# Kernel optimization log

Measured on AMD Instinct MI355X. Metric: run time of the kernel, lower is better.

The kernel has to match this reference:

```python
import jax, jax.numpy as jnp
import numpy as np

N_NODES = 100000
N_EDGES = 1600000
N_GRAPHS = 128
DIM = 64
N_LAYERS = 4
DENSE = 256
BN_EPS = 1e-5


def setup_inputs() -> dict:
    key = jax.random.key(0)
    ks = list(jax.random.split(key, 24))
    k = iter(ks)
    def lin(kk, fan_in, shape):
        b = 1.0 / np.sqrt(fan_in)
        return jax.random.uniform(kk, shape, jnp.float32, -b, b)
    inp = {}
    inp['x'] = jax.random.normal(next(k), (N_NODES, 32), jnp.float32)
    inp['edge_attr'] = jax.random.normal(next(k), (N_EDGES, 16), jnp.float32)
    inp['edge_index'] = jax.random.randint(next(k), (2, N_EDGES), 0, N_NODES, jnp.int32)
    inp['batch'] = jnp.sort(jax.random.randint(next(k), (N_NODES,), 0, N_GRAPHS, jnp.int32))
    # encoders
    inp['node_W'] = lin(next(k), 32, (32, DIM)); inp['node_b'] = lin(next(k), 32, (DIM,))
    inp['edge_W'] = lin(next(k), 16, (16, DIM)); inp['edge_b'] = lin(next(k), 16, (DIM,))
    # per-layer GINE MLPs (stacked over layer dim) and BN affine params
    inp['mlp1_W'] = lin(next(k), DIM, (N_LAYERS, DIM, DIM)); inp['mlp1_b'] = lin(next(k), DIM, (N_LAYERS, DIM))
    inp['mlp2_W'] = lin(next(k), DIM, (N_LAYERS, DIM, DIM)); inp['mlp2_b'] = lin(next(k), DIM, (N_LAYERS, DIM))
    inp['bn_gamma'] = jnp.ones((N_LAYERS, DIM), jnp.float32)
    inp['bn_beta'] = jnp.zeros((N_LAYERS, DIM), jnp.float32)
    # head: Linear(128,256) -> Linear(256,128) -> Linear(128,1)
    inp['head1_W'] = lin(next(k), 2 * DIM, (2 * DIM, DENSE)); inp['head1_b'] = lin(next(k), 2 * DIM, (DENSE,))
    inp['head2_W'] = lin(next(k), DENSE, (DENSE, DENSE // 2)); inp['head2_b'] = lin(next(k), DENSE, (DENSE // 2,))
    inp['head3_W'] = lin(next(k), DENSE // 2, (DENSE // 2, 1)); inp['head3_b'] = lin(next(k), DENSE // 2, (1,))
    return inp


def reference(x, edge_attr, edge_index, batch, node_W, node_b, edge_W, edge_b,
              mlp1_W, mlp1_b, mlp2_W, mlp2_b, bn_gamma, bn_beta,
              head1_W, head1_b, head2_W, head2_b, head3_W, head3_b):
    src, dst = edge_index[0], edge_index[1]  # messages flow src (x_j) -> dst (x_i)
    h = x @ node_W + node_b                  # [N, DIM]
    e = edge_attr @ edge_W + edge_b          # [E, DIM]
    for l in range(N_LAYERS):
        # GINEConv (eps = 0, not trained): mlp((1+eps)*x_i + sum_j relu(x_j + e_ij))
        msg = jax.nn.relu(h[src] + e)                              # [E, DIM]
        agg = jax.ops.segment_sum(msg, dst, num_segments=N_NODES)  # [N, DIM]
        z = h + agg
        z = jax.nn.relu(z @ mlp1_W[l] + mlp1_b[l]) @ mlp2_W[l] + mlp2_b[l]
        # BatchNorm1d (training-mode batch statistics, biased variance)
        mu = jnp.mean(z, axis=0)
        var = jnp.mean(jnp.square(z - mu), axis=0)
        z = (z - mu) * jax.lax.rsqrt(var + BN_EPS) * bn_gamma[l] + bn_beta[l]
        h = jax.nn.relu(z)
    sums = jax.ops.segment_sum(h, batch, num_segments=N_GRAPHS)                      # [G, DIM]
    counts = jax.ops.segment_sum(jnp.ones((h.shape[0],), h.dtype), batch, num_segments=N_GRAPHS)
    means = sums / jnp.maximum(counts, 1.0)[:, None]
    g = jnp.concatenate([sums, means], axis=1)   # [G, 2*DIM]
    g = jax.nn.relu(g @ head1_W + head1_b)       # dropout is identity at inference
    g = jax.nn.relu(g @ head2_W + head2_b)
    logits = (g @ head3_W + head3_b).reshape(-1) # [G]
    return logits
```

## Files before the change

### kernel.cpp

```cpp
#include <hip/hip_runtime.h>

#define SCAN_B 1024
#define NGRAPH 128
typedef unsigned short u16;
typedef unsigned int u32;
typedef u32 u32x2 __attribute__((ext_vector_type(2)));
typedef u32 u32x4 __attribute__((ext_vector_type(4)));
typedef float fx4 __attribute__((ext_vector_type(4)));
typedef _Float16 f16;
typedef _Float16 f16x2 __attribute__((ext_vector_type(2)));
typedef _Float16 f16x8 __attribute__((ext_vector_type(8)));
typedef float f32x4 __attribute__((ext_vector_type(4)));

__device__ __forceinline__ u16 f2h(float f) {
  f16 h = (f16)f;
  return __builtin_bit_cast(u16, h);
}
__device__ __forceinline__ float h2f(u16 u) {
  return (float)__builtin_bit_cast(f16, u);
}
__device__ __forceinline__ float hlo(u32 w) { return h2f((u16)(w & 0xffffu)); }
__device__ __forceinline__ float hhi(u32 w) { return h2f((u16)(w >> 16)); }

__device__ __forceinline__ void bn4(const float* __restrict__ stat,
                                    const float* __restrict__ gamma,
                                    const float* __restrict__ beta,
                                    float invN, int c4,
                                    float4& sc4, float4& sh4)
{
  float4 s1 = *(const float4*)&stat[c4];
  float4 s2 = *(const float4*)&stat[64 + c4];
  float4 g4 = *(const float4*)&gamma[c4];
  float4 b4 = *(const float4*)&beta[c4];
#define BN1(k)                                                        \
  { float mu = s1.k * invN;                                           \
    float var = fmaxf(s2.k * invN - mu * mu, 0.f);                    \
    sc4.k = g4.k * rsqrtf(var + 1e-5f);                               \
    sh4.k = b4.k - mu * sc4.k; }
  BN1(x) BN1(y) BN1(z) BN1(w)
#undef BN1
}

__global__ __launch_bounds__(256) void node_enc_kernel(
    const float* __restrict__ x, const float* __restrict__ W,
    const float* __restrict__ b, u16* __restrict__ zh, int N)
{
  int lane = threadIdx.x & 63;
  int wave = (blockIdx.x * blockDim.x + threadIdx.x) >> 6;
  int nw = (gridDim.x * blockDim.x) >> 6;
  float wcol[32];
#pragma unroll
  for (int k = 0; k < 32; ++k) wcol[k] = W[k * 64 + lane];
  float bb = b[lane];
  for (int n = wave; n < N; n += nw) {
    const fx4* xr = (const fx4*)(x + (size_t)n * 32);
    float acc = bb;
#pragma unroll
    for (int c = 0; c < 8; ++c) {
      fx4 v = __builtin_nontemporal_load(&xr[c]);
      acc = fmaf(v[0], wcol[4 * c + 0], acc);
      acc = fmaf(v[1], wcol[4 * c + 1], acc);
      acc = fmaf(v[2], wcol[4 * c + 2], acc);
      acc = fmaf(v[3], wcol[4 * c + 3], acc);
    }
    zh[(size_t)n * 64 + lane] = f2h(acc);
  }
}

__global__ __launch_bounds__(256) void count_pos_kernel(
    const int* __restrict__ dst, int* __restrict__ deg,
    int* __restrict__ pos, int E)
{
  int e = blockIdx.x * blockDim.x + threadIdx.x;
  if (e < E) pos[e] = atomicAdd(&deg[dst[e]], 1);
}

__global__ __launch_bounds__(SCAN_B) void scan1_kernel(
    const int* __restrict__ deg, int* __restrict__ rowp,
    int* __restrict__ bsum, int N)
{
  __shared__ int s[SCAN_B];
  int tid = threadIdx.x;
  int i = blockIdx.x * SCAN_B + tid;
  int v = (i < N) ? deg[i] : 0;
  s[tid] = v;
  __syncthreads();
  for (int off = 1; off < SCAN_B; off <<= 1) {
    int t = (tid >= off) ? s[tid - off] : 0;
    __syncthreads();
    s[tid] += t;
    __syncthreads();
  }
  if (i < N) rowp[i] = s[tid] - v;
  if (tid == SCAN_B - 1) bsum[blockIdx.x] = s[tid];
}

__global__ __launch_bounds__(128) void scan2_kernel(int* __restrict__ bsum, int NB)
{
  __shared__ int s[128];
  int tid = threadIdx.x;
  int v = (tid < NB) ? bsum[tid] : 0;
  s[tid] = v;
  __syncthreads();
  for (int off = 1; off < 128; off <<= 1) {
    int t = (tid >= off) ? s[tid - off] : 0;
    __syncthreads();
    s[tid] += t;
    __syncthreads();
  }
  if (tid < NB) bsum[tid] = s[tid] - v;
}

__global__ __launch_bounds__(SCAN_B) void scan3_kernel(
    int* __restrict__ rowp, const int* __restrict__ bsum, int N, int E)
{
  int i = blockIdx.x * SCAN_B + threadIdx.x;
  if (i < N) rowp[i] += bsum[blockIdx.x];
  if (i == 0) rowp[N] = E;
}

__global__ __launch_bounds__(256) void scatter_pos_kernel(
    const int* __restrict__ dst, const int* __restrict__ rowp,
    const int* __restrict__ pos, int* __restrict__ eids, int E)
{
  int e = blockIdx.x * blockDim.x + threadIdx.x;
  if (e >= E) return;
  int p = rowp[dst[e]] + pos[e];
  eids[p] = e;
}

__global__ __launch_bounds__(256) void scatter_e_kernel(
    const int* __restrict__ dst, const int* __restrict__ src,
    const int* __restrict__ pos, const fx4* __restrict__ attr4,
    const int* __restrict__ rowp, const float* __restrict__ eW,
    const float* __restrict__ eb_, int* __restrict__ src_s,
    u16* __restrict__ e_s, int E)
{
  int lane = threadIdx.x & 63;
  int c = lane & 15, q = lane >> 4;
  int wave = (blockIdx.x * blockDim.x + threadIdx.x) >> 6;
  int base = wave << 6;
  if (base >= E) return;
  int nb = E - base; if (nb > 64) nb = 64;

  float wcol[4][16];
#pragma unroll
  for (int ch = 0; ch < 4; ++ch)
#pragma unroll
    for (int k = 0; k < 16; ++k)
      wcol[ch][k] = eW[k * 64 + 4 * c + ch];
  float4 eb4 = *(const float4*)&eb_[4 * c];

  int pv = 0;
  if (lane < nb) {
    int e = base + lane;
    pv = rowp[dst[e]] + pos[e];
    src_s[pv] = src[e];
  }

  auto enc = [&](fx4 a0, fx4 a1, fx4 a2, fx4 a3, int slot) {
    float m0 = eb4.x, m1 = eb4.y, m2 = eb4.z, m3 = eb4.w;
#define ESTEP(av, k)                                                   \
    m0 = fmaf(av, wcol[0][k], m0); m1 = fmaf(av, wcol[1][k], m1);      \
    m2 = fmaf(av, wcol[2][k], m2); m3 = fmaf(av, wcol[3][k], m3);
    ESTEP(a0[0], 0)  ESTEP(a0[1], 1)  ESTEP(a0[2], 2)  ESTEP(a0[3], 3)
    ESTEP(a1[0], 4)  ESTEP(a1[1], 5)  ESTEP(a1[2], 6)  ESTEP(a1[3], 7)
    ESTEP(a2[0], 8)  ESTEP(a2[1], 9)  ESTEP(a2[2], 10) ESTEP(a2[3], 11)
    ESTEP(a3[0], 12) ESTEP(a3[1], 13) ESTEP(a3[2], 14) ESTEP(a3[3], 15)
#undef ESTEP
    u32x2 o;
    o[0] = (u32)f2h(m0) | ((u32)f2h(m1) << 16);
    o[1] = (u32)f2h(m2) | ((u32)f2h(m3) << 16);
    *(u32x2*)(e_s + (size_t)slot * 64 + 4 * c) = o;
  };

  if (nb == 64) {
#pragma unroll 2
    for (int t = 0; t < 16; t += 2) {
      int pA = __shfl(pv, 4 * t + q, 64);
      int pB = __shfl(pv, 4 * t + 4 + q, 64);
      const fx4* rA = attr4 + (size_t)(base + 4 * t + q) * 4;
      const fx4* rB = attr4 + (size_t)(base + 4 * t + 4 + q) * 4;
      fx4 A0 = __builtin_nontemporal_load(rA);
      fx4 A1 = __builtin_nontemporal_load(rA + 1);
      fx4 A2 = __builtin_nontemporal_load(rA + 2);
      fx4 A3 = __builtin_nontemporal_load(rA + 3);
      fx4 B0 = __builtin_nontemporal_load(rB);
      fx4 B1 = __builtin_nontemporal_load(rB + 1);
      fx4 B2 = __builtin_nontemporal_load(rB + 2);
      fx4 B3 = __builtin_nontemporal_load(rB + 3);
      enc(A0, A1, A2, A3, pA);
      enc(B0, B1, B2, B3, pB);
    }
  } else {
    for (int t = 0; 4 * t < nb; ++t) {
      int idx = 4 * t + q;
      int p = __shfl(pv, idx < nb ? idx : 0, 64);
      if (idx < nb) {
        const fx4* rA = attr4 + (size_t)(base + idx) * 4;
        fx4 A0 = rA[0], A1 = rA[1], A2 = rA[2], A3 = rA[3];
        enc(A0, A1, A2, A3, p);
      }
    }
  }
}

__global__ __launch_bounds__(256) void prep_weights_kernel(
    const float* __restrict__ mlp1_W, const float* __restrict__ mlp2_W,
    u16* __restrict__ Wt)
{
  int idx = blockIdx.x * 256 + threadIdx.x;
  if (idx >= 32768) return;
  int layer = idx >> 13;
  int which = (idx >> 12) & 1;
  int d = (idx >> 6) & 63;
  int k = idx & 63;
  const float* W = which ? mlp2_W : mlp1_W;
  Wt[idx] = f2h(W[layer * 4096 + k * 64 + d]);
}

__global__ __launch_bounds__(256, 4) void gather_kernel(
    const u16* __restrict__ zh, const float* __restrict__ stat_rd,
    const float* __restrict__ gamma, const float* __restrict__ beta,
    float invN, float* __restrict__ stat_wr,
    const u16* __restrict__ e_s, const int* __restrict__ srcv,
    const int* __restrict__ rowp, u16* __restrict__ gh, int N)
{
  if (blockIdx.x == 0 && threadIdx.x < 128) stat_wr[threadIdx.x] = 0.f;

  int lane = threadIdx.x & 63;
  int c = lane & 15, q = lane >> 4;
  int wave = (blockIdx.x * blockDim.x + threadIdx.x) >> 6;
  int nw = (gridDim.x * blockDim.x) >> 6;

  const bool ubn = stat_rd != nullptr;
  float4 sc4 = make_float4(1.f, 1.f, 1.f, 1.f);
  float4 sh4 = make_float4(0.f, 0.f, 0.f, 0.f);
  if (ubn) bn4(stat_rd, gamma, beta, invN, 4 * c, sc4, sh4);

  auto hval4 = [&](u32x2 z, float& h0, float& h1, float& h2, float& h3) {
    h0 = hlo(z[0]); h1 = hhi(z[0]); h2 = hlo(z[1]); h3 = hhi(z[1]);
    if (ubn) {
      h0 = fmaxf(fmaf(h0, sc4.x, sh4.x), 0.f);
      h1 = fmaxf(fmaf(h1, sc4.y, sh4.y), 0.f);
      h2 = fmaxf(fmaf(h2, sc4.z, sh4.z), 0.f);
      h3 = fmaxf(fmaf(h3, sc4.w, sh4.w), 0.f);
    }
  };
  auto body = [&](u32x2 z, u32x2 e,
                  float& A0, float& A1, float& A2, float& A3) {
    float h0, h1, h2, h3;
    hval4(z, h0, h1, h2, h3);
    A0 += fmaxf(h0 + hlo(e[0]), 0.f);
    A1 += fmaxf(h1 + hhi(e[0]), 0.f);
    A2 += fmaxf(h2 + hlo(e[1]), 0.f);
    A3 += fmaxf(h3 + hhi(e[1]), 0.f);
  };

  for (int node = wave; node < N; node += nw) {
    const int j0 = rowp[node], j1 = rowp[node + 1];
    float acc0 = 0.f, acc1 = 0.f, acc2 = 0.f, acc3 = 0.f;

    for (int base = j0; base < j1; base += 64) {
      int nb = j1 - base; if (nb > 64) nb = 64;
      int iv = (lane < nb) ? srcv[base + lane] : 0;
      int ng = nb >> 2;
      int t = 0;
      for (; t + 4 <= ng; t += 4) {
        int s0 = __shfl(iv, 4 * t + q, 64);
        int s1 = __shfl(iv, 4 * t + 4 + q, 64);
        int s2 = __shfl(iv, 4 * t + 8 + q, 64);
        int s3 = __shfl(iv, 4 * t + 12 + q, 64);
        u32x2 z0 = *(const u32x2*)(zh + (size_t)s0 * 64 + 4 * c);
        u32x2 z1 = *(const u32x2*)(zh + (size_t)s1 * 64 + 4 * c);
        u32x2 z2 = *(const u32x2*)(zh + (size_t)s2 * 64 + 4 * c);
        u32x2 z3 = *(const u32x2*)(zh + (size_t)s3 * 64 + 4 * c);
        u32x2 e0 = *(const u32x2*)(e_s + (size_t)(base + 4 * t + q) * 64 + 4 * c);
        u32x2 e1 = *(const u32x2*)(e_s + (size_t)(base + 4 * t + 4 + q) * 64 + 4 * c);
        u32x2 e2 = *(const u32x2*)(e_s + (size_t)(base + 4 * t + 8 + q) * 64 + 4 * c);
        u32x2 e3 = *(const u32x2*)(e_s + (size_t)(base + 4 * t + 12 + q) * 64 + 4 * c);
        body(z0, e0, acc0, acc1, acc2, acc3);
        body(z1, e1, acc0, acc1, acc2, acc3);
        body(z2, e2, acc0, acc1, acc2, acc3);
        body(z3, e3, acc0, acc1, acc2, acc3);
      }
      for (; t < ng; ++t) {
        int s0 = __shfl(iv, 4 * t + q, 64);
        u32x2 z0 = *(const u32x2*)(zh + (size_t)s0 * 64 + 4 * c);
        u32x2 e0 = *(const u32x2*)(e_s + (size_t)(base + 4 * t + q) * 64 + 4 * c);
        body(z0, e0, acc0, acc1, acc2, acc3);
      }
      int tail = nb & 3;
      if (tail) {
        int idx = 4 * ng + (q < tail ? q : 0);
        int s0 = __shfl(iv, idx, 64);
        u32x2 z0 = *(const u32x2*)(zh + (size_t)s0 * 64 + 4 * c);
        u32x2 e0 = *(const u32x2*)(e_s + (size_t)(base + idx) * 64 + 4 * c);
        float h0, h1, h2, h3;
        hval4(z0, h0, h1, h2, h3);
        float wmask = (q < tail) ? 1.f : 0.f;
        acc0 += wmask * fmaxf(h0 + hlo(e0[0]), 0.f);
        acc1 += wmask * fmaxf(h1 + hhi(e0[0]), 0.f);
        acc2 += wmask * fmaxf(h2 + hlo(e0[1]), 0.f);
        acc3 += wmask * fmaxf(h3 + hhi(e0[1]), 0.f);
      }
    }
    acc0 += __shfl_xor(acc0, 16, 64); acc0 += __shfl_xor(acc0, 32, 64);
    acc1 += __shfl_xor(acc1, 16, 64); acc1 += __shfl_xor(acc1, 32, 64);
    acc2 += __shfl_xor(acc2, 16, 64); acc2 += __shfl_xor(acc2, 32, 64);
    acc3 += __shfl_xor(acc3, 16, 64); acc3 += __shfl_xor(acc3, 32, 64);
    if (q == 0) {
      u32x2 zn = *(const u32x2*)(zh + (size_t)node * 64 + 4 * c);
      float h0, h1, h2, h3;
      hval4(zn, h0, h1, h2, h3);
      acc0 += h0; acc1 += h1; acc2 += h2; acc3 += h3;
      u32x2 o;
      o[0] = (u32)f2h(acc0) | ((u32)f2h(acc1) << 16);
      o[1] = (u32)f2h(acc2) | ((u32)f2h(acc3) << 16);
      *(u32x2*)(gh + (size_t)node * 64 + 4 * c) = o;
    }
  }
}

__global__ __launch_bounds__(256) void gather_fallback_kernel(
    const u16* __restrict__ zh, const float* __restrict__ stat_rd,
    const float* __restrict__ gamma, const float* __restrict__ beta,
    float invN, float* __restrict__ stat_wr,
    const int* __restrict__ srcv, const int* __restrict__ eids,
    const int* __restrict__ rowp, const float* __restrict__ attr,
    const float* __restrict__ eW, const float* __restrict__ eb_,
    u16* __restrict__ gh, int N)
{
  if (blockIdx.x == 0 && threadIdx.x < 128) stat_wr[threadIdx.x] = 0.f;
  int lane = threadIdx.x & 63;
  int node = (blockIdx.x * blockDim.x + threadIdx.x) >> 6;
  if (node >= N) return;
  const bool ubn = stat_rd != nullptr;
  float sc = 1.f, sh = 0.f;
  if (ubn) {
    float mu = stat_rd[lane] * invN;
    float var = fmaxf(stat_rd[64 + lane] * invN - mu * mu, 0.f);
    sc = gamma[lane] * rsqrtf(var + 1e-5f);
    sh = beta[lane] - mu * sc;
  }
  auto hval = [&](float zz) -> float {
    float v = fmaf(zz, sc, sh);
    return ubn ? fmaxf(v, 0.f) : v;
  };
  float wcol[16];
#pragma unroll
  for (int k = 0; k < 16; ++k) wcol[k] = eW[k * 64 + lane];
  float eb = eb_[lane];
  const int j0 = rowp[node], j1 = rowp[node + 1];
  float acc = hval(h2f(zh[(size_t)node * 64 + lane]));
  for (int j = j0; j < j1; ++j) {
    int eid = eids[j];
    int s = srcv[j];
    const float4* ar = (const float4*)(attr + (size_t)eid * 16);
    float4 a0 = ar[0], a1 = ar[1], a2 = ar[2], a3 = ar[3];
    float m = eb;
    m = fmaf(a0.x, wcol[0], m);  m = fmaf(a0.y, wcol[1], m);
    m = fmaf(a0.z, wcol[2], m);  m = fmaf(a0.w, wcol[3], m);
    m = fmaf(a1.x, wcol[4], m);  m = fmaf(a1.y, wcol[5], m);
    m = fmaf(a1.z, wcol[6], m);  m = fmaf(a1.w, wcol[7], m);
    m = fmaf(a2.x, wcol[8], m);  m = fmaf(a2.y, wcol[9], m);
    m = fmaf(a2.z, wcol[10], m); m = fmaf(a2.w, wcol[11], m);
    m = fmaf(a3.x, wcol[12], m); m = fmaf(a3.y, wcol[13], m);
    m = fmaf(a3.z, wcol[14], m); m = fmaf(a3.w, wcol[15], m);
    acc += fmaxf(hval(h2f(zh[(size_t)s * 64 + lane])) + m, 0.f);
  }
  gh[(size_t)node * 64 + lane] = f2h(acc);
}

__global__ __launch_bounds__(256) void mlp_mfma_kernel(
    const u16* __restrict__ gh, u16* __restrict__ zh,
    const u16* __restrict__ W1t, const u16* __restrict__ W2t,
    const float* __restrict__ b1, const float* __restrict__ b2,
    float* __restrict__ stat, int N)
{
  __shared__ __align__(16) u16 ylds[4][16][72];
  __shared__ float sstat[128];
  int tid = threadIdx.x, lane = tid & 63, w = tid >> 6;
  int l15 = lane & 15, lg = lane >> 4;
  int row_base = (blockIdx.x * 4 + w) * 32;

  if (tid < 128) sstat[tid] = 0.f;
  __syncthreads();

  f16x8 w1f[2][4], w2f[2][4];
#pragma unroll
  for (int ks = 0; ks < 2; ++ks)
#pragma unroll
    for (int nt = 0; nt < 4; ++nt) {
      int off = (nt * 16 + l15) * 64 + ks * 32 + lg * 8;
      w1f[ks][nt] = *(const f16x8*)&W1t[off];
      w2f[ks][nt] = *(const f16x8*)&W2t[off];
    }
  float bv1[4], bv2[4];
#pragma unroll
  for (int nt = 0; nt < 4; ++nt) {
    bv1[nt] = b1[nt * 16 + l15];
    bv2[nt] = b2[nt * 16 + l15];
  }

  float s1acc[4] = {0.f, 0.f, 0.f, 0.f};
  float s2acc[4] = {0.f, 0.f, 0.f, 0.f};

#pragma unroll
  for (int tile = 0; tile < 2; ++tile) {
    int grow0 = row_base + tile * 16;
    int arow = grow0 + l15; if (arow >= N) arow = N - 1;
    const u16* grow = gh + (size_t)arow * 64;
    f16x8 a0 = *(const f16x8*)(grow + lg * 8);
    f16x8 a1 = *(const f16x8*)(grow + 32 + lg * 8);

    f32x4 c1[4];
#pragma unroll
    for (int nt = 0; nt < 4; ++nt) {
      c1[nt] = (f32x4){0.f, 0.f, 0.f, 0.f};
      c1[nt] = __builtin_amdgcn_mfma_f32_16x16x32_f16(a0, w1f[0][nt], c1[nt], 0, 0, 0);
      c1[nt] = __builtin_amdgcn_mfma_f32_16x16x32_f16(a1, w1f[1][nt], c1[nt], 0, 0, 0);
    }
#pragma unroll
    for (int nt = 0; nt < 4; ++nt)
#pragma unroll
      for (int r = 0; r < 4; ++r)
        ylds[w][lg * 4 + r][nt * 16 + l15] = f2h(fmaxf(c1[nt][r] + bv1[nt], 0.f));
    f16x8 a20 = *(const f16x8*)&ylds[w][l15][lg * 8];
    f16x8 a21 = *(const f16x8*)&ylds[w][l15][32 + lg * 8];

    f32x4 c2[4];
#pragma unroll
    for (int nt = 0; nt < 4; ++nt) {
      c2[nt] = (f32x4){0.f, 0.f, 0.f, 0.f};
      c2[nt] = __builtin_amdgcn_mfma_f32_16x16x32_f16(a20, w2f[0][nt], c2[nt], 0, 0, 0);
      c2[nt] = __builtin_amdgcn_mfma_f32_16x16x32_f16(a21, w2f[1][nt], c2[nt], 0, 0, 0);
    }
#pragma unroll
    for (int nt = 0; nt < 4; ++nt) {
#pragma unroll
      for (int r = 0; r < 4; ++r) {
        int row = grow0 + lg * 4 + r;
        float v = c2[nt][r] + bv2[nt];
        bool ok = row < N;
        if (ok) zh[(size_t)row * 64 + nt * 16 + l15] = f2h(v);
        float vm = ok ? v : 0.f;
        s1acc[nt] += vm;
        s2acc[nt] = fmaf(vm, vm, s2acc[nt]);
      }
    }
  }

#pragma unroll
  for (int nt = 0; nt < 4; ++nt) {
    float s1 = s1acc[nt], s2 = s2acc[nt];
    s1 += __shfl_xor(s1, 16, 64); s1 += __shfl_xor(s1, 32, 64);
    s2 += __shfl_xor(s2, 16, 64); s2 += __shfl_xor(s2, 32, 64);
    if (lg == 0) {
      atomicAdd(&sstat[nt * 16 + l15], s1);
      atomicAdd(&sstat[64 + nt * 16 + l15], s2);
    }
  }
  __syncthreads();
  if (tid < 128) atomicAdd(&stat[tid], sstat[tid]);
}

__global__ __launch_bounds__(256) void pool_kernel(
    const u16* __restrict__ zh, const float* __restrict__ stat_rd,
    const float* __restrict__ gamma, const float* __restrict__ beta,
    float invN, const int* __restrict__ batch,
    float* __restrict__ sums, float* __restrict__ cnts, int N)
{
  int lane = threadIdx.x & 63;
  int wave = (blockIdx.x * blockDim.x + threadIdx.x) >> 6;
  int r0 = wave * 64;
  if (r0 >= N) return;
  float mu = stat_rd[lane] * invN;
  float var = fmaxf(stat_rd[64 + lane] * invN - mu * mu, 0.f);
  float sc = gamma[lane] * rsqrtf(var + 1e-5f);
  float sh = beta[lane] - mu * sc;
  int r1 = min(r0 + 64, N);
  int cur = batch[r0];
  float acc = 0.f;
  int cnt = 0;
  for (int r = r0; r < r1; ++r) {
    int bg = batch[r];
    if (bg != cur) {
      atomicAdd(&sums[(size_t)cur * 64 + lane], acc);
      if (lane == 0) atomicAdd(&cnts[cur], (float)cnt);
      acc = 0.f; cnt = 0; cur = bg;
    }
    acc += fmaxf(fmaf(h2f(zh[(size_t)r * 64 + lane]), sc, sh), 0.f);
    cnt++;
  }
  atomicAdd(&sums[(size_t)cur * 64 + lane], acc);
  if (lane == 0) atomicAdd(&cnts[cur], (float)cnt);
}

__global__ __launch_bounds__(256) void head_kernel(
    const float* __restrict__ sums, const float* __restrict__ cnts,
    const float* __restrict__ W1, const float* __restrict__ b1,
    const float* __restrict__ W2, const float* __restrict__ b2,
    const float* __restrict__ W3, const float* __restrict__ b3,
    float* __restrict__ out)
{
  __shared__ float gf[128];
  __shared__ float h1s[256];
  __shared__ float h2s[128];
  int g = blockIdx.x, t = threadIdx.x;
  if (t < 64) {
    float sv = sums[(size_t)g * 64 + t];
    gf[t] = sv;
    gf[64 + t] = sv / fmaxf(cnts[g], 1.f);
  }
  __syncthreads();
  float a = b1[t];
  for (int k = 0; k < 128; ++k) a = fmaf(gf[k], W1[k * 256 + t], a);
  h1s[t] = fmaxf(a, 0.f);
  __syncthreads();
  if (t < 128) {
    float a2 = b2[t];
    for (int k = 0; k < 256; ++k) a2 = fmaf(h1s[k], W2[k * 128 + t], a2);
    h2s[t] = fmaxf(a2, 0.f);
  }
  __syncthreads();
  if (t == 0) {
    float s = b3[0];
    for (int k = 0; k < 128; ++k) s = fmaf(h2s[k], W3[k], s);
    out[g] = s;
  }
}

extern "C" void kernel_launch(void* const* d_in, const int* in_sizes, int n_in,
                              void* d_out, int out_size, void* d_ws, size_t ws_size,
                              hipStream_t stream)
{
  const float* x         = (const float*)d_in[0];
  const float* edge_attr = (const float*)d_in[1];
  const int*   ei        = (const int*)  d_in[2];
  const int*   batch     = (const int*)  d_in[3];
  const float* node_W    = (const float*)d_in[4];
  const float* node_b    = (const float*)d_in[5];
  const float* edge_W    = (const float*)d_in[6];
  const float* edge_b    = (const float*)d_in[7];
  const float* mlp1_W    = (const float*)d_in[8];
  const float* mlp1_b    = (const float*)d_in[9];
  const float* mlp2_W    = (const float*)d_in[10];
  const float* mlp2_b    = (const float*)d_in[11];
  const float* bn_gamma  = (const float*)d_in[12];
  const float* bn_beta   = (const float*)d_in[13];
  const float* head1_W   = (const float*)d_in[14];
  const float* head1_b   = (const float*)d_in[15];
  const float* head2_W   = (const float*)d_in[16];
  const float* head2_b   = (const float*)d_in[17];
  const float* head3_W   = (const float*)d_in[18];
  const float* head3_b   = (const float*)d_in[19];
  float* out = (float*)d_out;
  (void)n_in; (void)out_size;

  const int N = in_sizes[0] / 32;
  const int E = in_sizes[2] / 2;
  const int* srcp = ei;
  const int* dstp = ei + E;

  auto al = [](size_t b) { return (b + 255) & ~(size_t)255; };
  const size_t sz_zh   = al((size_t)N * 64 * 2);
  const size_t sz_g    = al((size_t)N * 64 * 2);
  const size_t sz_es   = al((size_t)E * 64 * 2);
  const size_t sz_src  = al((size_t)E * 4);
  const size_t sz_pos  = al((size_t)E * 4);
  const size_t sz_eids = al((size_t)E * 4);
  const size_t sz_rowp = al((size_t)(N + 1) * 4);
  const size_t sz_wt   = al(32768 * 2);
  const size_t sz_scr  = al((size_t)N * 4);
  const size_t sz_small = al(512) * 3 + al(NGRAPH * 64 * 4) + al(NGRAPH * 4);

  const size_t need_sorted = sz_zh + sz_g + sz_es + sz_src + sz_pos +
                             sz_eids + sz_rowp + sz_wt + sz_scr + sz_small;
  const bool sorted = ws_size >= need_sorted;

  char* p = (char*)d_ws;
  auto take = [&](size_t b) -> char* { char* q = p; p += b; return q; };

  u16*   zh   = (u16*)  take(sz_zh);
  u16*   gh   = (u16*)  take(sz_g);
  int*   rowp = (int*)  take(sz_rowp);
  u16*   Wt   = (u16*)  take(sz_wt);
  float* statA= (float*)take(al(512));
  float* statB= (float*)take(al(512));
  int*   bsum = (int*)  take(al(512));
  float* sums = (float*)take(al(NGRAPH * 64 * 4));
  float* cnts = (float*)take(al(NGRAPH * 4));
  int*   deg  = (int*)  take(sz_scr);
  int*   pos  = (int*)  take(sz_pos);
  int*   eids = (int*)  take(sz_eids);
  int*   src_s= (int*)  take(sz_src);

  u16* e_s = nullptr;
  if (sorted) e_s = (u16*)take(sz_es);

  const int NB = (N + SCAN_B - 1) / SCAN_B;
  const float invN = 1.0f / (float)N;
  float* statbuf[2] = {statA, statB};

  hipMemsetAsync(deg, 0, (size_t)N * 4, stream);

  node_enc_kernel<<<2048, 256, 0, stream>>>(x, node_W, node_b, zh, N);
  prep_weights_kernel<<<128, 256, 0, stream>>>(mlp1_W, mlp2_W, Wt);
  count_pos_kernel<<<(E + 255) / 256, 256, 0, stream>>>(dstp, deg, pos, E);
  scan1_kernel<<<NB, SCAN_B, 0, stream>>>(deg, rowp, bsum, N);
  scan2_kernel<<<1, 128, 0, stream>>>(bsum, NB);
  scan3_kernel<<<NB, SCAN_B, 0, stream>>>(rowp, bsum, N, E);
  if (sorted) {
    scatter_e_kernel<<<(E + 255) / 256, 256, 0, stream>>>(
        dstp, srcp, pos, (const fx4*)edge_attr, rowp, edge_W, edge_b,
        src_s, e_s, E);
  } else {
    scatter_pos_kernel<<<(E + 255) / 256, 256, 0, stream>>>(
        dstp, rowp, pos, eids, E);
    scatter_e_kernel<<<(E + 255) / 256, 256, 0, stream>>>(
        dstp, srcp, pos, (const fx4*)edge_attr, rowp, edge_W, edge_b,
        src_s, nullptr, E);
  }

  const int mlpBlocks = (N + 127) / 128;
  for (int l = 0; l < 4; ++l) {
    const float* stat_rd = (l == 0) ? nullptr : statbuf[(l - 1) & 1];
    float* stat_wr = statbuf[l & 1];
    const float* gma = bn_gamma + (size_t)(l ? (l - 1) : 0) * 64;
    const float* bta = bn_beta + (size_t)(l ? (l - 1) : 0) * 64;
    if (sorted) {
      gather_kernel<<<4096, 256, 0, stream>>>(
          zh, stat_rd, gma, bta, invN, stat_wr, e_s, src_s, rowp, gh, N);
    } else {
      gather_fallback_kernel<<<(N + 3) / 4, 256, 0, stream>>>(
          zh, stat_rd, gma, bta, invN, stat_wr, src_s, eids, rowp,
          edge_attr, edge_W, edge_b, gh, N);
    }
    mlp_mfma_kernel<<<mlpBlocks, 256, 0, stream>>>(
        gh, zh, Wt + (size_t)l * 8192, Wt + (size_t)l * 8192 + 4096,
        mlp1_b + (size_t)l * 64, mlp2_b + (size_t)l * 64, stat_wr, N);
  }

  hipMemsetAsync(sums, 0, (size_t)NGRAPH * 64 * 4, stream);
  hipMemsetAsync(cnts, 0, (size_t)NGRAPH * 4, stream);
  const int poolWaves = (N + 63) / 64;
  pool_kernel<<<(poolWaves + 3) / 4, 256, 0, stream>>>(
      zh, statbuf[1], bn_gamma + 3 * 64, bn_beta + 3 * 64, invN,
      batch, sums, cnts, N);
  head_kernel<<<NGRAPH, 256, 0, stream>>>(
      sums, cnts, head1_W, head1_b, head2_W, head2_b, head3_W, head3_b, out);
}
```

Measured before the change: 739.0 us.

## Store encoded edges in natural order and gather them via sorted (src, eid) pairs

Encoded edge features are now written in original edge order by a coalesced encode kernel, instead of being scattered into dst-sorted slots. A separate kernel scatters (src, edge id) pairs into CSR order. The gather kernel then reads edge features indirectly through the edge id. This makes the one-time encode write contiguous, but turns the per-layer edge-feature reads, run four times, from contiguous streaming into random 128-byte row gathers. It also doubles the size of the index array read in each layer.

New measurement: 733.3 us. No clear change (-0.8%).

```diff
diff --git a/kernel.cpp b/kernel.cpp
--- a/kernel.cpp
+++ b/kernel.cpp
@@ -7,8 +7,8 @@
 typedef u32 u32x2 __attribute__((ext_vector_type(2)));
 typedef u32 u32x4 __attribute__((ext_vector_type(4)));
 typedef float fx4 __attribute__((ext_vector_type(4)));
+typedef int ix2 __attribute__((ext_vector_type(2)));
 typedef _Float16 f16;
-typedef _Float16 f16x2 __attribute__((ext_vector_type(2)));
 typedef _Float16 f16x8 __attribute__((ext_vector_type(8)));
 typedef float f32x4 __attribute__((ext_vector_type(4)));
 
@@ -119,29 +119,27 @@
   if (i == 0) rowp[N] = E;
 }
 
-__global__ __launch_bounds__(256) void scatter_pos_kernel(
-    const int* __restrict__ dst, const int* __restrict__ rowp,
-    const int* __restrict__ pos, int* __restrict__ eids, int E)
+__global__ __launch_bounds__(256) void scatter_pairs_kernel(
+    const int* __restrict__ dst, const int* __restrict__ src,
+    const int* __restrict__ pos, const int* __restrict__ rowp,
+    ix2* __restrict__ pairs, int E)
 {
   int e = blockIdx.x * blockDim.x + threadIdx.x;
   if (e >= E) return;
   int p = rowp[dst[e]] + pos[e];
-  eids[p] = e;
-}
-
-__global__ __launch_bounds__(256) void scatter_e_kernel(
-    const int* __restrict__ dst, const int* __restrict__ src,
-    const int* __restrict__ pos, const fx4* __restrict__ attr4,
-    const int* __restrict__ rowp, const float* __restrict__ eW,
-    const float* __restrict__ eb_, int* __restrict__ src_s,
-    u16* __restrict__ e_s, int E)
+  ix2 v; v[0] = src[e]; v[1] = e;
+  pairs[p] = v;
+}
+
+__global__ __launch_bounds__(256) void encode_kernel(
+    const fx4* __restrict__ attr4, const float* __restrict__ eW,
+    const float* __restrict__ eb_, u16* __restrict__ e_nat, int E)
 {
   int lane = threadIdx.x & 63;
   int c = lane & 15, q = lane >> 4;
   int wave = (blockIdx.x * blockDim.x + threadIdx.x) >> 6;
   int base = wave << 6;
   if (base >= E) return;
-  int nb = E - base; if (nb > 64) nb = 64;
 
   float wcol[4][16];
 #pragma unroll
@@ -151,14 +149,7 @@
       wcol[ch][k] = eW[k * 64 + 4 * c + ch];
   float4 eb4 = *(const float4*)&eb_[4 * c];
 
-  int pv = 0;
-  if (lane < nb) {
-    int e = base + lane;
-    pv = rowp[dst[e]] + pos[e];
-    src_s[pv] = src[e];
-  }
-
-  auto enc = [&](fx4 a0, fx4 a1, fx4 a2, fx4 a3, int slot) {
+  auto enc = [&](fx4 a0, fx4 a1, fx4 a2, fx4 a3, int edge) {
     float m0 = eb4.x, m1 = eb4.y, m2 = eb4.z, m3 = eb4.w;
 #define ESTEP(av, k)                                                   \
     m0 = fmaf(av, wcol[0][k], m0); m1 = fmaf(av, wcol[1][k], m1);      \
@@ -171,35 +162,28 @@
     u32x2 o;
     o[0] = (u32)f2h(m0) | ((u32)f2h(m1) << 16);
     o[1] = (u32)f2h(m2) | ((u32)f2h(m3) << 16);
-    *(u32x2*)(e_s + (size_t)slot * 64 + 4 * c) = o;
+    *(u32x2*)(e_nat + (size_t)edge * 64 + 4 * c) = o;
   };
 
+  int nb = E - base; if (nb > 64) nb = 64;
   if (nb == 64) {
 #pragma unroll 2
-    for (int t = 0; t < 16; t += 2) {
-      int pA = __shfl(pv, 4 * t + q, 64);
-      int pB = __shfl(pv, 4 * t + 4 + q, 64);
-      const fx4* rA = attr4 + (size_t)(base + 4 * t + q) * 4;
-      const fx4* rB = attr4 + (size_t)(base + 4 * t + 4 + q) * 4;
+    for (int t = 0; t < 16; ++t) {
+      int edge = base + 4 * t + q;
+      const fx4* rA = attr4 + (size_t)edge * 4;
       fx4 A0 = __builtin_nontemporal_load(rA);
       fx4 A1 = __builtin_nontemporal_load(rA + 1);
       fx4 A2 = __builtin_nontemporal_load(rA + 2);
       fx4 A3 = __builtin_nontemporal_load(rA + 3);
-      fx4 B0 = __builtin_nontemporal_load(rB);
-      fx4 B1 = __builtin_nontemporal_load(rB + 1);
-      fx4 B2 = __builtin_nontemporal_load(rB + 2);
-      fx4 B3 = __builtin_nontemporal_load(rB + 3);
-      enc(A0, A1, A2, A3, pA);
-      enc(B0, B1, B2, B3, pB);
+      enc(A0, A1, A2, A3, edge);
     }
   } else {
     for (int t = 0; 4 * t < nb; ++t) {
-      int idx = 4 * t + q;
-      int p = __shfl(pv, idx < nb ? idx : 0, 64);
-      if (idx < nb) {
-        const fx4* rA = attr4 + (size_t)(base + idx) * 4;
+      int edge = base + 4 * t + q;
+      if (edge < E && 4 * t + q < nb) {
+        const fx4* rA = attr4 + (size_t)edge * 4;
         fx4 A0 = rA[0], A1 = rA[1], A2 = rA[2], A3 = rA[3];
-        enc(A0, A1, A2, A3, p);
+        enc(A0, A1, A2, A3, edge);
       }
     }
   }
@@ -223,7 +207,7 @@
     const u16* __restrict__ zh, const float* __restrict__ stat_rd,
     const float* __restrict__ gamma, const float* __restrict__ beta,
     float invN, float* __restrict__ stat_wr,
-    const u16* __restrict__ e_s, const int* __restrict__ srcv,
+    const u16* __restrict__ e_nat, const ix2* __restrict__ pairs,
     const int* __restrict__ rowp, u16* __restrict__ gh, int N)
 {
   if (blockIdx.x == 0 && threadIdx.x < 128) stat_wr[threadIdx.x] = 0.f;
@@ -263,39 +247,47 @@
 
     for (int base = j0; base < j1; base += 64) {
       int nb = j1 - base; if (nb > 64) nb = 64;
-      int iv = (lane < nb) ? srcv[base + lane] : 0;
+      ix2 iv = {0, 0};
+      if (lane < nb) iv = pairs[base + lane];
+      int sv = iv[0], dv = iv[1];
       int ng = nb >> 2;
       int t = 0;
       for (; t + 4 <= ng; t += 4) {
-        int s0 = __shfl(iv, 4 * t + q, 64);
-        int s1 = __shfl(iv, 4 * t + 4 + q, 64);
-        int s2 = __shfl(iv, 4 * t + 8 + q, 64);
-        int s3 = __shfl(iv, 4 * t + 12 + q, 64);
+        int s0 = __shfl(sv, 4 * t + q, 64);
+        int s1 = __shfl(sv, 4 * t + 4 + q, 64);
+        int s2 = __shfl(sv, 4 * t + 8 + q, 64);
+        int s3 = __shfl(sv, 4 * t + 12 + q, 64);
+        int d0 = __shfl(dv, 4 * t + q, 64);
+        int d1 = __shfl(dv, 4 * t + 4 + q, 64);
+        int d2 = __shfl(dv, 4 * t + 8 + q, 64);
+        int d3 = __shfl(dv, 4 * t + 12 + q, 64);
         u32x2 z0 = *(const u32x2*)(zh + (size_t)s0 * 64 + 4 * c);
         u32x2 z1 = *(const u32x2*)(zh + (size_t)s1 * 64 + 4 * c);
         u32x2 z2 = *(const u32x2*)(zh + (size_t)s2 * 64 + 4 * c);
         u32x2 z3 = *(const u32x2*)(zh + (size_t)s3 * 64 + 4 * c);
-        u32x2 e0 = *(const u32x2*)(e_s + (size_t)(base + 4 * t + q) * 64 + 4 * c);
-        u32x2 e1 = *(const u32x2*)(e_s + (size_t)(base + 4 * t + 4 + q) * 64 + 4 * c);
-        u32x2 e2 = *(const u32x2*)(e_s + (size_t)(base + 4 * t + 8 + q) * 64 + 4 * c);
-        u32x2 e3 = *(const u32x2*)(e_s + (size_t)(base + 4 * t + 12 + q) * 64 + 4 * c);
+        u32x2 e0 = *(const u32x2*)(e_nat + (size_t)d0 * 64 + 4 * c);
+        u32x2 e1 = *(const u32x2*)(e_nat + (size_t)d1 * 64 + 4 * c);
+        u32x2 e2 = *(const u32x2*)(e_nat + (size_t)d2 * 64 + 4 * c);
+        u32x2 e3 = *(const u32x2*)(e_nat + (size_t)d3 * 64 + 4 * c);
         body(z0, e0, acc0, acc1, acc2, acc3);
         body(z1, e1, acc0, acc1, acc2, acc3);
         body(z2, e2, acc0, acc1, acc2, acc3);
         body(z3, e3, acc0, acc1, acc2, acc3);
       }
       for (; t < ng; ++t) {
-        int s0 = __shfl(iv, 4 * t + q, 64);
+        int s0 = __shfl(sv, 4 * t + q, 64);
+        int d0 = __shfl(dv, 4 * t + q, 64);
         u32x2 z0 = *(const u32x2*)(zh + (size_t)s0 * 64 + 4 * c);
-        u32x2 e0 = *(const u32x2*)(e_s + (size_t)(base + 4 * t + q) * 64 + 4 * c);
+        u32x2 e0 = *(const u32x2*)(e_nat + (size_t)d0 * 64 + 4 * c);
         body(z0, e0, acc0, acc1, acc2, acc3);
       }
       int tail = nb & 3;
       if (tail) {
         int idx = 4 * ng + (q < tail ? q : 0);
-        int s0 = __shfl(iv, idx, 64);
+        int s0 = __shfl(sv, idx, 64);
+        int d0 = __shfl(dv, idx, 64);
         u32x2 z0 = *(const u32x2*)(zh + (size_t)s0 * 64 + 4 * c);
-        u32x2 e0 = *(const u32x2*)(e_s + (size_t)(base + idx) * 64 + 4 * c);
+        u32x2 e0 = *(const u32x2*)(e_nat + (size_t)d0 * 64 + 4 * c);
         float h0, h1, h2, h3;
         hval4(z0, h0, h1, h2, h3);
         float wmask = (q < tail) ? 1.f : 0.f;
@@ -326,10 +318,9 @@
     const u16* __restrict__ zh, const float* __restrict__ stat_rd,
     const float* __restrict__ gamma, const float* __restrict__ beta,
     float invN, float* __restrict__ stat_wr,
-    const int* __restrict__ srcv, const int* __restrict__ eids,
-    const int* __restrict__ rowp, const float* __restrict__ attr,
-    const float* __restrict__ eW, const float* __restrict__ eb_,
-    u16* __restrict__ gh, int N)
+    const ix2* __restrict__ pairs, const int* __restrict__ rowp,
+    const float* __restrict__ attr, const float* __restrict__ eW,
+    const float* __restrict__ eb_, u16* __restrict__ gh, int N)
 {
   if (blockIdx.x == 0 && threadIdx.x < 128) stat_wr[threadIdx.x] = 0.f;
   int lane = threadIdx.x & 63;
@@ -354,8 +345,8 @@
   const int j0 = rowp[node], j1 = rowp[node + 1];
   float acc = hval(h2f(zh[(size_t)node * 64 + lane]));
   for (int j = j0; j < j1; ++j) {
-    int eid = eids[j];
-    int s = srcv[j];
+    ix2 pr = pairs[j];
+    int s = pr[0], eid = pr[1];
     const float4* ar = (const float4*)(attr + (size_t)eid * 16);
     float4 a0 = ar[0], a1 = ar[1], a2 = ar[2], a3 = ar[3];
     float m = eb;
@@ -564,40 +555,38 @@
   const int* dstp = ei + E;
 
   auto al = [](size_t b) { return (b + 255) & ~(size_t)255; };
-  const size_t sz_zh   = al((size_t)N * 64 * 2);
-  const size_t sz_g    = al((size_t)N * 64 * 2);
-  const size_t sz_es   = al((size_t)E * 64 * 2);
-  const size_t sz_src  = al((size_t)E * 4);
-  const size_t sz_pos  = al((size_t)E * 4);
-  const size_t sz_eids = al((size_t)E * 4);
-  const size_t sz_rowp = al((size_t)(N + 1) * 4);
-  const size_t sz_wt   = al(32768 * 2);
-  const size_t sz_scr  = al((size_t)N * 4);
+  const size_t sz_zh    = al((size_t)N * 64 * 2);
+  const size_t sz_g     = al((size_t)N * 64 * 2);
+  const size_t sz_en    = al((size_t)E * 64 * 2);
+  const size_t sz_pairs = al((size_t)E * 8);
+  const size_t sz_pos   = al((size_t)E * 4);
+  const size_t sz_rowp  = al((size_t)(N + 1) * 4);
+  const size_t sz_wt    = al(32768 * 2);
+  const size_t sz_scr   = al((size_t)N * 4);
   const size_t sz_small = al(512) * 3 + al(NGRAPH * 64 * 4) + al(NGRAPH * 4);
 
-  const size_t need_sorted = sz_zh + sz_g + sz_es + sz_src + sz_pos +
-                             sz_eids + sz_rowp + sz_wt + sz_scr + sz_small;
+  const size_t need_sorted = sz_zh + sz_g + sz_en + sz_pairs + sz_pos +
+                             sz_rowp + sz_wt + sz_scr + sz_small;
   const bool sorted = ws_size >= need_sorted;
 
   char* p = (char*)d_ws;
   auto take = [&](size_t b) -> char* { char* q = p; p += b; return q; };
 
-  u16*   zh   = (u16*)  take(sz_zh);
-  u16*   gh   = (u16*)  take(sz_g);
-  int*   rowp = (int*)  take(sz_rowp);
-  u16*   Wt   = (u16*)  take(sz_wt);
-  float* statA= (float*)take(al(512));
-  float* statB= (float*)take(al(512));
-  int*   bsum = (int*)  take(al(512));
-  float* sums = (float*)take(al(NGRAPH * 64 * 4));
-  float* cnts = (float*)take(al(NGRAPH * 4));
-  int*   deg  = (int*)  take(sz_scr);
-  int*   pos  = (int*)  take(sz_pos);
-  int*   eids = (int*)  take(sz_eids);
-  int*   src_s= (int*)  take(sz_src);
-
-  u16* e_s = nullptr;
-  if (sorted) e_s = (u16*)take(sz_es);
+  u16*   zh    = (u16*)  take(sz_zh);
+  u16*   gh    = (u16*)  take(sz_g);
+  int*   rowp  = (int*)  take(sz_rowp);
+  u16*   Wt    = (u16*)  take(sz_wt);
+  float* statA = (float*)take(al(512));
+  float* statB = (float*)take(al(512));
+  int*   bsum  = (int*)  take(al(512));
+  float* sums  = (float*)take(al(NGRAPH * 64 * 4));
+  float* cnts  = (float*)take(al(NGRAPH * 4));
+  int*   deg   = (int*)  take(sz_scr);
+  int*   pos   = (int*)  take(sz_pos);
+  ix2*   pairs = (ix2*)  take(sz_pairs);
+
+  u16* e_nat = nullptr;
+  if (sorted) e_nat = (u16*)take(sz_en);
 
   const int NB = (N + SCAN_B - 1) / SCAN_B;
   const float invN = 1.0f / (float)N;
@@ -611,16 +600,11 @@
   scan1_kernel<<<NB, SCAN_B, 0, stream>>>(deg, rowp, bsum, N);
   scan2_kernel<<<1, 128, 0, stream>>>(bsum, NB);
   scan3_kernel<<<NB, SCAN_B, 0, stream>>>(rowp, bsum, N, E);
+  scatter_pairs_kernel<<<(E + 255) / 256, 256, 0, stream>>>(
+      dstp, srcp, pos, rowp, pairs, E);
   if (sorted) {
-    scatter_e_kernel<<<(E + 255) / 256, 256, 0, stream>>>(
-        dstp, srcp, pos, (const fx4*)edge_attr, rowp, edge_W, edge_b,
-        src_s, e_s, E);
-  } else {
-    scatter_pos_kernel<<<(E + 255) / 256, 256, 0, stream>>>(
-        dstp, rowp, pos, eids, E);
-    scatter_e_kernel<<<(E + 255) / 256, 256, 0, stream>>>(
-        dstp, srcp, pos, (const fx4*)edge_attr, rowp, edge_W, edge_b,
-        src_s, nullptr, E);
+    encode_kernel<<<(E + 255) / 256, 256, 0, stream>>>(
+        (const fx4*)edge_attr, edge_W, edge_b, e_nat, E);
   }
 
   const int mlpBlocks = (N + 127) / 128;
@@ -631,10 +615,10 @@
     const float* bta = bn_beta + (size_t)(l ? (l - 1) : 0) * 64;
     if (sorted) {
       gather_kernel<<<4096, 256, 0, stream>>>(
-          zh, stat_rd, gma, bta, invN, stat_wr, e_s, src_s, rowp, gh, N);
+          zh, stat_rd, gma, bta, invN, stat_wr, e_nat, pairs, rowp, gh, N);
     } else {
       gather_fallback_kernel<<<(N + 3) / 4, 256, 0, stream>>>(
-          zh, stat_rd, gma, bta, invN, stat_wr, src_s, eids, rowp,
+          zh, stat_rd, gma, bta, invN, stat_wr, pairs, rowp,
           edge_attr, edge_W, edge_b, gh, N);
     }
     mlp_mfma_kernel<<<mlpBlocks, 256, 0, stream>>>(
```
